# Kernel tuning notes

Hardware: AMD Instinct MI355X
Metric: run time of the kernel (lower is better)

Reference implementation:

```python
import jax, jax.numpy as jnp
import numpy as np

N = 65536   # voxels
K = 27      # 3x3x3 kernel offsets
LOG_P = float(np.log(101.0))  # Hmax = log(num img channels)
EPS_BN = 1e-5


def bn(x, p):
    # p: [4, C] = (gamma, beta, running_mean, running_var); eval-mode batchnorm
    g, b, m, v = p[0], p[1], p[2], p[3]
    return g * (x - m) * jax.lax.rsqrt(v + EPS_BN) + b


def spconv(x, nbr, W):
    # sparse 3^3 conv as gather-GEMM: x [N,Cin], nbr [N,K] int, W [K,Cin,Cout]
    g = x[nbr]                       # [N, K, Cin] irregular gather
    return jnp.einsum('nkc,kcd->nd', g, W)


def setup_inputs() -> dict:
    key = jax.random.key(0)
    ks = jax.random.split(key, 24)
    inp = {
        'feats': jax.random.uniform(ks[0], (N, 105), dtype=jnp.float32),
        'nbr1': jax.random.randint(ks[1], (N, K), 0, N, dtype=jnp.int32),
        'nbr2': jax.random.randint(ks[2], (N, K), 0, N, dtype=jnp.int32),
        'w_rgb': jax.random.normal(ks[3], (4, 32), jnp.float32) * 0.1,
        'b_rgb': jax.random.normal(ks[4], (32,), jnp.float32) * 0.1,
        'bn_rgb': jax.random.uniform(ks[5], (4, 32), dtype=jnp.float32),
        'w_img': jax.random.normal(ks[6], (101, 32), jnp.float32) * 0.1,
        'b_img': jax.random.normal(ks[7], (32,), jnp.float32) * 0.1,
        'bn_img': jax.random.uniform(ks[8], (4, 32), dtype=jnp.float32),
        'w_e1': jax.random.normal(ks[9], (K, 64, 96), jnp.float32) * 0.05,
        'w_e2': jax.random.normal(ks[10], (K, 96, 96), jnp.float32) * 0.05,
        'bn_e1': jax.random.uniform(ks[11], (4, 96), dtype=jnp.float32),
        'bn_e2': jax.random.uniform(ks[12], (4, 96), dtype=jnp.float32),
        'w_lab': jax.random.normal(ks[13], (96, 19), jnp.float32) * 0.1,
        'w_unlab': jax.random.normal(ks[14], (5, 96, 5), jnp.float32) * 0.1,
        'w_over': jax.random.normal(ks[15], (5, 96, 15), jnp.float32) * 0.1,
        'w_clip1': jax.random.normal(ks[16], (96, 256), jnp.float32) * 0.1,
        'b_clip1': jax.random.normal(ks[17], (256,), jnp.float32) * 0.1,
        'bn_clip': jax.random.uniform(ks[18], (4, 256), dtype=jnp.float32),
        'w_clip2': jax.random.normal(ks[19], (256, 512), jnp.float32) * 0.1,
        'b_clip2': jax.random.normal(ks[20], (512,), jnp.float32) * 0.1,
    }
    return inp


def reference(feats, nbr1, nbr2, w_rgb, b_rgb, bn_rgb, w_img, b_img, bn_img,
              w_e1, w_e2, bn_e1, bn_e2, w_lab, w_unlab, w_over,
              w_clip1, b_clip1, bn_clip, w_clip2, b_clip2):
    rgbi = feats[:, :4]
    p = feats[:, 4:]
    # entropy gate (computed under no_grad in the original)
    p_safe = jnp.clip(p, 1e-12, None)
    H = -(p_safe * jnp.log(p_safe)).sum(axis=1, keepdims=True)
    w = jax.lax.stop_gradient(1.0 - H / LOG_P)
    p_gate = p * w  # eval mode: no dropout
    # 1x1 sparse convs = per-voxel matmuls
    rgb32 = jax.nn.relu(bn(rgbi @ w_rgb + b_rgb, bn_rgb))
    img32 = jax.nn.relu(bn(p_gate @ w_img + b_img, bn_img))
    x = jnp.concatenate([rgb32, img32], axis=1)  # [N, 64]
    # encoder: gather-GEMM sparse 3^3 convs (MinkUNet body pattern), 64->96->96
    x = jax.nn.relu(bn(spconv(x, nbr1, w_e1), bn_e1))
    x = jax.nn.relu(bn(spconv(x, nbr2, w_e2), bn_e2))  # [N, 96] = feats
    # prototype heads (1x1 convs, bias-free)
    logits_lab = x @ w_lab                                 # [N, 19]
    logits_unlab = jnp.einsum('nc,hcp->hnp', x, w_unlab)   # [5, N, 5]
    logits_over = jnp.einsum('nc,hcp->hnp', x, w_over)     # [5, N, 15]
    # clip projector
    h = jax.nn.relu(bn(x @ w_clip1 + b_clip1, bn_clip))
    clip_feats = h @ w_clip2 + b_clip2                     # [N, 512]
    return (logits_lab, logits_unlab, logits_over, x, clip_feats)
```

## Files before the change

### kernel.cpp

```cpp
#include <hip/hip_runtime.h>
#include <math.h>

#define NNODES 65536
#define KNBR 27
#define EPS_BN 1e-5f
#define LOG_P 4.6151205168412597f

typedef float f32x4 __attribute__((ext_vector_type(4)));
typedef short s16x8 __attribute__((ext_vector_type(8)));

__device__ __forceinline__ unsigned short f2bf(float f) {
    union { float f; unsigned int u; } v; v.f = f;
    unsigned int u = v.u;
    unsigned int r = (u + 0x7fffu + ((u >> 16) & 1u)) >> 16;
    return (unsigned short)r;
}

__device__ __forceinline__ void gload16(const void* g, void* l) {
    __builtin_amdgcn_global_load_lds(
        (const __attribute__((address_space(1))) void*)g,
        (__attribute__((address_space(3))) void*)l, 16, 0, 0);
}

__global__ __launch_bounds__(256) void prep_w_kernel(
    const float* __restrict__ W, unsigned short* __restrict__ wpre, int CIN, int NCH)
{
    const int idx = blockIdx.x * 256 + threadIdx.x;
    const int total = KNBR * 96 * NCH * 8;
    if (idx >= total) return;
    const int e  = idx & 7;
    const int t1 = idx >> 3;
    const int ci = t1 % NCH;
    const int t2 = t1 / NCH;
    const int r  = t2 % 96;
    const int k  = t2 / 96;
    const int cc  = ci ^ (r & (NCH - 1));
    const int cin = cc * 8 + e;
    float v = (cin < CIN) ? W[((size_t)k * CIN + cin) * 96 + r] : 0.f;
    wpre[idx] = f2bf(v);
}

__global__ __launch_bounds__(256) void prep_wc1h_kernel(
    const float* __restrict__ w_clip1, const float* __restrict__ w_lab,
    const float* __restrict__ w_unlab, const float* __restrict__ w_over,
    unsigned short* __restrict__ out)
{
    const int idx = blockIdx.x * 256 + threadIdx.x;
    if (idx >= 3 * 384 * 32) return;
    const int e   = idx & 7;
    const int p2  = (idx >> 3) & 3;
    const int col = (idx >> 5) % 384;
    const int kt  = (idx >> 5) / 384;
    const int cin = (kt * 4 + (p2 ^ ((col >> 2) & 3))) * 8 + e;
    float v;
    if (col < 256)      v = w_clip1[(size_t)cin * 256 + col];
    else if (col < 275) v = w_lab[(size_t)cin * 19 + (col - 256)];
    else if (col < 300) { int jj = col - 275, hh = jj / 5,  p = jj - hh * 5;  v = w_unlab[((size_t)hh * 96 + cin) * 5  + p]; }
    else if (col < 375) { int jj = col - 300, hh = jj / 15, p = jj - hh * 15; v = w_over [((size_t)hh * 96 + cin) * 15 + p]; }
    else v = 0.f;
    out[idx] = f2bf(v);
}

__global__ __launch_bounds__(256) void prep_wc2_kernel(
    const float* __restrict__ w_clip2, unsigned short* __restrict__ out)
{
    const int idx = blockIdx.x * 256 + threadIdx.x;
    const int e   = idx & 7;
    const int p2  = (idx >> 3) & 3;
    const int col = (idx >> 5) & 511;
    const int kt  = idx >> 14;
    const int cin = (kt * 4 + (p2 ^ ((col >> 2) & 3))) * 8 + e;
    out[idx] = f2bf(w_clip2[(size_t)cin * 512 + col]);
}

__global__ __launch_bounds__(256) void stage1_kernel(
    const float* __restrict__ feats,
    const float* __restrict__ w_rgb, const float* __restrict__ b_rgb, const float* __restrict__ bn_rgb,
    const float* __restrict__ w_img, const float* __restrict__ b_img, const float* __restrict__ bn_img,
    unsigned short* __restrict__ x64b)
{
    __shared__ float s_f[4][106];
    const int wid  = threadIdx.x >> 6;
    const int lane = threadIdx.x & 63;
    const int n = blockIdx.x * 4 + wid;
    const float* fr = feats + (size_t)n * 105;
    for (int i = lane; i < 105; i += 64) s_f[wid][i] = fr[i];
    __syncthreads();

    float s = 0.f;
    for (int i = lane; i < 101; i += 64) {
        float pv = s_f[wid][4 + i];
        float ps = fmaxf(pv, 1e-12f);
        s += ps * logf(ps);
    }
    #pragma unroll
    for (int off = 32; off > 0; off >>= 1) s += __shfl_xor(s, off, 64);
    const float wgt = 1.0f + s * (1.0f / LOG_P);

    if (lane < 32) {
        const int j = lane;
        float acc = b_rgb[j];
        #pragma unroll
        for (int c = 0; c < 4; ++c) acc += s_f[wid][c] * w_rgb[c*32 + j];
        float y = bn_rgb[j] * (acc - bn_rgb[64+j]) * rsqrtf(bn_rgb[96+j] + EPS_BN) + bn_rgb[32+j];
        x64b[(size_t)n*64 + j] = f2bf(fmaxf(y, 0.f));
    } else {
        const int j = lane - 32;
        float acc = 0.f;
        for (int c = 0; c < 101; ++c) acc += s_f[wid][4+c] * w_img[c*32 + j];
        acc = acc * wgt + b_img[j];
        float y = bn_img[j] * (acc - bn_img[64+j]) * rsqrtf(bn_img[96+j] + EPS_BN) + bn_img[32+j];
        x64b[(size_t)n*64 + 32 + j] = f2bf(fmaxf(y, 0.f));
    }
}

template<int CIN, bool OUTBF>
__global__ __launch_bounds__(256, 2) void spconv_mfma(
    const char* __restrict__ xinb,
    const int*  __restrict__ nbr,
    const char* __restrict__ wpre,
    const float* __restrict__ bnp,
    float* __restrict__ outf,
    unsigned short* __restrict__ outb)
{
    constexpr int KT   = CIN / 32;
    constexpr int NCH  = (CIN == 96) ? 16 : 8;
    constexpr int CM   = NCH - 1;
    constexpr int ROWB = NCH * 16;
    constexpr int STG  = (96 * ROWB) / 4096;

    __shared__ int s_nbr[128 * KNBR];
    __shared__ __align__(16) char s_b[2][96 * ROWB];

    const int t   = threadIdx.x;
    const int wid = t >> 6;
    const int l   = t & 63;
    const int l15 = l & 15;
    const int l4  = l >> 4;
    const int n0  = blockIdx.x * 128;

    for (int i = t; i < 128 * KNBR; i += 256) s_nbr[i] = nbr[(size_t)n0 * KNBR + i];

    f32x4 acc[2][6];
    #pragma unroll
    for (int mt = 0; mt < 2; ++mt)
        #pragma unroll
        for (int nt = 0; nt < 6; ++nt) acc[mt][nt] = (f32x4){0.f, 0.f, 0.f, 0.f};

    float sc[6], mb[6], bb[6];
    #pragma unroll
    for (int nt = 0; nt < 6; ++nt) {
        const int d = nt * 16 + l15;
        sc[nt] = bnp[d] * rsqrtf(bnp[288 + d] + EPS_BN);
        mb[nt] = bnp[192 + d];
        bb[nt] = bnp[96 + d];
    }

    s16x8 a0[2][KT], a1[2][KT], a2r[2][KT];

#define STAGE(kk) do {                                                         \
    const char* _src = wpre + (size_t)(kk) * (96 * ROWB);                      \
    char* _dst = &s_b[(kk) & 1][0];                                            \
    _Pragma("unroll")                                                          \
    for (int _i = 0; _i < STG; ++_i)                                           \
        gload16(_src + _i * 4096 + t * 16, _dst + _i * 4096 + (wid << 10));    \
} while (0)

#define PRE(areg, kk) do {                                                     \
    _Pragma("unroll")                                                          \
    for (int _mt = 0; _mt < 2; ++_mt) {                                        \
        const int _nb = s_nbr[(wid * 32 + _mt * 16 + l15) * KNBR + (kk)];      \
        const char* _rp = xinb + (size_t)_nb * (CIN * 2) + (l4 << 4);          \
        _Pragma("unroll")                                                      \
        for (int _kt = 0; _kt < KT; ++_kt)                                     \
            areg[_mt][_kt] = *(const s16x8*)(_rp + _kt * 64);                  \
    }                                                                          \
} while (0)

#define COMP(areg, kk) do {                                                    \
    const char* _bb = &s_b[(kk) & 1][0];                                       \
    _Pragma("unroll")                                                          \
    for (int _kt = 0; _kt < KT; ++_kt) {                                       \
        s16x8 _bf[6];                                                          \
        _Pragma("unroll")                                                      \
        for (int _nt = 0; _nt < 6; ++_nt) {                                    \
            const int _row = _nt * 16 + l15;                                   \
            const int _c   = _kt * 4 + l4;                                     \
            _bf[_nt] = *(const s16x8*)(_bb + _row * ROWB + ((_c ^ (_row & CM)) << 4)); \
        }                                                                      \
        _Pragma("unroll")                                                      \
        for (int _nt = 0; _nt < 6; ++_nt) {                                    \
            acc[0][_nt] = __builtin_amdgcn_mfma_f32_16x16x32_bf16(areg[0][_kt], _bf[_nt], acc[0][_nt], 0, 0, 0); \
            acc[1][_nt] = __builtin_amdgcn_mfma_f32_16x16x32_bf16(areg[1][_kt], _bf[_nt], acc[1][_nt], 0, 0, 0); \
        }                                                                      \
    }                                                                          \
} while (0)

    __syncthreads();
    PRE(a0, 0);
    PRE(a1, 1);
    STAGE(0);
    __syncthreads();

    for (int k = 0; k < 27; k += 3) {
        STAGE(k + 1);
        PRE(a2r, k + 2);
        COMP(a0, k);
        __syncthreads();
        STAGE(k + 2);
        if (k + 3 < 27) PRE(a0, k + 3);
        COMP(a1, k + 1);
        __syncthreads();
        if (k + 3 < 27) STAGE(k + 3);
        if (k + 4 < 27) PRE(a1, k + 4);
        COMP(a2r, k + 2);
        __syncthreads();
    }

#undef STAGE
#undef PRE
#undef COMP

    #pragma unroll
    for (int mt = 0; mt < 2; ++mt)
        #pragma unroll
        for (int nt = 0; nt < 6; ++nt) {
            const int d = nt * 16 + l15;
            #pragma unroll
            for (int q = 0; q < 4; ++q) {
                const int node = n0 + wid * 32 + mt * 16 + l4 * 4 + q;
                float y = sc[nt] * (acc[mt][nt][q] - mb[nt]) + bb[nt];
                y = fmaxf(y, 0.f);
                if (OUTBF) outb[(size_t)node * 96 + d] = f2bf(y);
                else       outf[(size_t)node * 96 + d] = y;
            }
        }
}

__global__ __launch_bounds__(512, 2) void fused_clip_heads(
    const float* __restrict__ x,
    const char* __restrict__ wc1h,
    const char* __restrict__ wc2,
    const float* __restrict__ b_clip1, const float* __restrict__ bn_clip,
    const float* __restrict__ b_clip2,
    float* __restrict__ out_lab, float* __restrict__ out_unlab, float* __restrict__ out_over,
    float* __restrict__ outc)
{
    extern __shared__ __align__(16) char lds[];
    char* reg0 = lds;
    char* s_h  = lds + 65536;

    const int t   = threadIdx.x;
    const int wid = t >> 6;
    const int l   = t & 63;
    const int l15 = l & 15;
    const int l4  = l >> 4;
    const int wm  = wid >> 2;
    const int wn  = wid & 3;
    const int r0  = blockIdx.x * 128;

#define STG1(kt) do {                                                          \
    const char* _s = wc1h + (size_t)(kt) * 24576;                              \
    char* _d = reg0 + ((kt) & 1) * 32768;                                      \
    _Pragma("unroll")                                                          \
    for (int _i = 0; _i < 3; ++_i)                                             \
        gload16(_s + _i * 8192 + t * 16, _d + _i * 8192 + (wid << 10));        \
} while (0)

#define STG2(kt) do {                                                          \
    const char* _s = wc2 + (size_t)(kt) * 32768;                               \
    char* _d = reg0 + ((kt) & 1) * 32768;                                      \
    _Pragma("unroll")                                                          \
    for (int _i = 0; _i < 4; ++_i)                                             \
        gload16(_s + _i * 8192 + t * 16, _d + _i * 8192 + (wid << 10));        \
} while (0)

    STG1(0);

    s16x8 af[3][4];
    #pragma unroll
    for (int kt = 0; kt < 3; ++kt)
        #pragma unroll
        for (int mt = 0; mt < 4; ++mt) {
            const int r = r0 + wm*64 + mt*16 + l15;
            const float* bp = x + (size_t)r*96 + kt*32 + l4*8;
            const float4 xa = *(const float4*)bp;
            const float4 xb = *(const float4*)(bp + 4);
            s16x8 v;
            v[0]=(short)f2bf(xa.x); v[1]=(short)f2bf(xa.y); v[2]=(short)f2bf(xa.z); v[3]=(short)f2bf(xa.w);
            v[4]=(short)f2bf(xb.x); v[5]=(short)f2bf(xb.y); v[6]=(short)f2bf(xb.z); v[7]=(short)f2bf(xb.w);
            af[kt][mt] = v;
        }

    f32x4 acc1[4][6];
    #pragma unroll
    for (int mt = 0; mt < 4; ++mt)
        #pragma unroll
        for (int nt = 0; nt < 6; ++nt) acc1[mt][nt] = (f32x4){0.f,0.f,0.f,0.f};

    __syncthreads();

    for (int kt = 0; kt < 3; ++kt) {
        if (kt < 2) STG1(kt + 1);
        const char* buf = reg0 + (kt & 1) * 32768;
        s16x8 bf[6];
        #pragma unroll
        for (int nt = 0; nt < 6; ++nt) {
            const int col = wn*96 + nt*16 + l15;
            bf[nt] = *(const s16x8*)(buf + col*64 + ((l4 ^ ((col >> 2) & 3)) << 4));
        }
        #pragma unroll
        for (int nt = 0; nt < 6; ++nt)
            #pragma unroll
            for (int mt = 0; mt < 4; ++mt)
                acc1[mt][nt] = __builtin_amdgcn_mfma_f32_16x16x32_bf16(af[kt][mt], bf[nt], acc1[mt][nt], 0, 0, 0);
        __syncthreads();
    }

    STG2(0);

    #pragma unroll
    for (int nt = 0; nt < 6; ++nt) {
        const int j = wn*96 + nt*16 + l15;
        if (j < 256) {
            const float sc = bn_clip[j] * rsqrtf(bn_clip[768 + j] + EPS_BN);
            const float mb = bn_clip[512 + j];
            const float bb = bn_clip[256 + j];
            const float bias = b_clip1[j];
            const int c = j >> 3, e = j & 7;
            #pragma unroll
            for (int mt = 0; mt < 4; ++mt)
                #pragma unroll
                for (int q = 0; q < 4; ++q) {
                    const int row = wm*64 + mt*16 + l4*4 + q;
                    float y = fmaxf(sc * (acc1[mt][nt][q] + bias - mb) + bb, 0.f);
                    *(unsigned short*)(s_h + row*512 + ((c ^ (row & 31)) << 4) + e*2) = f2bf(y);
                }
        } else if (j < 375) {
            const int jh = j - 256;
            #pragma unroll
            for (int mt = 0; mt < 4; ++mt)
                #pragma unroll
                for (int q = 0; q < 4; ++q) {
                    const int n = r0 + wm*64 + mt*16 + l4*4 + q;
                    const float v = acc1[mt][nt][q];
                    if (jh < 19)      out_lab[(size_t)n*19 + jh] = v;
                    else if (jh < 44) { int jj = jh-19, hh = jj/5,  p = jj-hh*5;  out_unlab[((size_t)hh*NNODES + n)*5  + p] = v; }
                    else              { int jj = jh-44, hh = jj/15, p = jj-hh*15; out_over [((size_t)hh*NNODES + n)*15 + p] = v; }
                }
        }
    }
    __syncthreads();

    f32x4 acc2[4][8];
    #pragma unroll
    for (int mt = 0; mt < 4; ++mt)
        #pragma unroll
        for (int nt = 0; nt < 8; ++nt) acc2[mt][nt] = (f32x4){0.f,0.f,0.f,0.f};

    for (int kt = 0; kt < 8; ++kt) {
        if (kt < 7) STG2(kt + 1);
        const char* buf = reg0 + (kt & 1) * 32768;
        s16x8 a2[4];
        #pragma unroll
        for (int mt = 0; mt < 4; ++mt) {
            const int row = wm*64 + mt*16 + l15;
            a2[mt] = *(const s16x8*)(s_h + row*512 + (((kt*4 + l4) ^ (row & 31)) << 4));
        }
        s16x8 b2[8];
        #pragma unroll
        for (int nt = 0; nt < 8; ++nt) {
            const int col = wn*128 + nt*16 + l15;
            b2[nt] = *(const s16x8*)(buf + col*64 + ((l4 ^ ((col >> 2) & 3)) << 4));
        }
        #pragma unroll
        for (int nt = 0; nt < 8; ++nt)
            #pragma unroll
            for (int mt = 0; mt < 4; ++mt)
                acc2[mt][nt] = __builtin_amdgcn_mfma_f32_16x16x32_bf16(a2[mt], b2[nt], acc2[mt][nt], 0, 0, 0);
        __syncthreads();
    }
#undef STG1
#undef STG2

    #pragma unroll
    for (int nt = 0; nt < 8; ++nt) {
        const int col = wn*128 + nt*16 + l15;
        const float bb = b_clip2[col];
        #pragma unroll
        for (int mt = 0; mt < 4; ++mt)
            #pragma unroll
            for (int q = 0; q < 4; ++q) {
                const int row = wm*64 + mt*16 + l4*4 + q;
                outc[(size_t)(r0 + row)*512 + col] = acc2[mt][nt][q] + bb;
            }
    }
}

extern "C" void kernel_launch(void* const* d_in, const int* in_sizes, int n_in,
                              void* d_out, int out_size, void* d_ws, size_t ws_size,
                              hipStream_t stream)
{
    const float* feats   = (const float*)d_in[0];
    const int*   nbr1    = (const int*)  d_in[1];
    const int*   nbr2    = (const int*)  d_in[2];
    const float* w_rgb   = (const float*)d_in[3];
    const float* b_rgb   = (const float*)d_in[4];
    const float* bn_rgb  = (const float*)d_in[5];
    const float* w_img   = (const float*)d_in[6];
    const float* b_img   = (const float*)d_in[7];
    const float* bn_img  = (const float*)d_in[8];
    const float* w_e1    = (const float*)d_in[9];
    const float* w_e2    = (const float*)d_in[10];
    const float* bn_e1   = (const float*)d_in[11];
    const float* bn_e2   = (const float*)d_in[12];
    const float* w_lab   = (const float*)d_in[13];
    const float* w_unlab = (const float*)d_in[14];
    const float* w_over  = (const float*)d_in[15];
    const float* w_clip1 = (const float*)d_in[16];
    const float* b_clip1 = (const float*)d_in[17];
    const float* bn_clip = (const float*)d_in[18];
    const float* w_clip2 = (const float*)d_in[19];
    const float* b_clip2 = (const float*)d_in[20];

    float* out = (float*)d_out;
    const size_t off_unlab = (size_t)NNODES * 19;
    const size_t off_over  = (size_t)NNODES * 44;
    const size_t off_x     = (size_t)NNODES * 119;
    const size_t off_clip  = (size_t)NNODES * 215;

    char* scratch = (char*)(out + off_clip);
    unsigned short* x64b  = (unsigned short*)scratch;
    unsigned short* x96b  = (unsigned short*)(scratch + (8u << 20));
    unsigned short* wpre1 = (unsigned short*)(scratch + (21u << 20));
    unsigned short* wpre2 = (unsigned short*)(scratch + (22u << 20));

    char* wc1h = (char*)d_ws;
    char* wc2  = (char*)d_ws + 73728;

    prep_w_kernel<<<(KNBR*96*8*8  + 255) / 256, 256, 0, stream>>>(w_e1, wpre1, 64, 8);
    prep_w_kernel<<<(KNBR*96*16*8 + 255) / 256, 256, 0, stream>>>(w_e2, wpre2, 96, 16);
    prep_wc1h_kernel<<<(3*384*32 + 255) / 256, 256, 0, stream>>>(w_clip1, w_lab, w_unlab, w_over,
                                                                 (unsigned short*)wc1h);
    prep_wc2_kernel<<<131072 / 256, 256, 0, stream>>>(w_clip2, (unsigned short*)wc2);

    stage1_kernel<<<NNODES/4, 256, 0, stream>>>(feats, w_rgb, b_rgb, bn_rgb, w_img, b_img, bn_img, x64b);

    spconv_mfma<64, true ><<<NNODES/128, 256, 0, stream>>>((const char*)x64b, nbr1, (const char*)wpre1,
                                                           bn_e1, nullptr, x96b);
    spconv_mfma<96, false><<<NNODES/128, 256, 0, stream>>>((const char*)x96b, nbr2, (const char*)wpre2,
                                                           bn_e2, out + off_x, nullptr);

    fused_clip_heads<<<NNODES/128, 512, 131072, stream>>>(
        out + off_x, wc1h, wc2, b_clip1, bn_clip, b_clip2,
        out, out + off_unlab, out + off_over, out + off_clip);
}
```

Before: 252.4 us.

## Halve spconv rows per wave, drop LDS neighbor table, raise occupancy

Each wave in the sparse-conv kernels now covers 16 voxels instead of 32, so a block handles 64 rows and twice as many blocks are launched. The LDS neighbor-index table is removed and each PRE reads its index straight from global memory. BN constants are now loaded in the epilogue instead of being held in registers, and launch bounds allow 3 blocks per CU. The smaller register and LDS footprint is meant to raise occupancy and hide gather latency. In exchange, each staged weight tile in LDS is reused by half as many rows, which doubles weight staging traffic per voxel.

```diff
diff --git a/kernel.cpp b/kernel.cpp
--- a/kernel.cpp
+++ b/kernel.cpp
@@ -115,7 +115,7 @@
 }
 
 template<int CIN, bool OUTBF>
-__global__ __launch_bounds__(256, 2) void spconv_mfma(
+__global__ __launch_bounds__(256, 3) void spconv_mfma(
     const char* __restrict__ xinb,
     const int*  __restrict__ nbr,
     const char* __restrict__ wpre,
@@ -129,7 +129,6 @@
     constexpr int ROWB = NCH * 16;
     constexpr int STG  = (96 * ROWB) / 4096;
 
-    __shared__ int s_nbr[128 * KNBR];
     __shared__ __align__(16) char s_b[2][96 * ROWB];
 
     const int t   = threadIdx.x;
@@ -137,26 +136,14 @@
     const int l   = t & 63;
     const int l15 = l & 15;
     const int l4  = l >> 4;
-    const int n0  = blockIdx.x * 128;
-
-    for (int i = t; i < 128 * KNBR; i += 256) s_nbr[i] = nbr[(size_t)n0 * KNBR + i];
-
-    f32x4 acc[2][6];
-    #pragma unroll
-    for (int mt = 0; mt < 2; ++mt)
-        #pragma unroll
-        for (int nt = 0; nt < 6; ++nt) acc[mt][nt] = (f32x4){0.f, 0.f, 0.f, 0.f};
-
-    float sc[6], mb[6], bb[6];
-    #pragma unroll
-    for (int nt = 0; nt < 6; ++nt) {
-        const int d = nt * 16 + l15;
-        sc[nt] = bnp[d] * rsqrtf(bnp[288 + d] + EPS_BN);
-        mb[nt] = bnp[192 + d];
-        bb[nt] = bnp[96 + d];
-    }
-
-    s16x8 a0[2][KT], a1[2][KT], a2r[2][KT];
+    const int n0  = blockIdx.x * 64;
+    const size_t nbase = (size_t)(n0 + wid * 16 + l15) * KNBR;
+
+    f32x4 acc[6];
+    #pragma unroll
+    for (int nt = 0; nt < 6; ++nt) acc[nt] = (f32x4){0.f, 0.f, 0.f, 0.f};
+
+    s16x8 a0[KT], a1[KT], a2r[KT];
 
 #define STAGE(kk) do {                                                         \
     const char* _src = wpre + (size_t)(kk) * (96 * ROWB);                      \
@@ -167,14 +154,11 @@
 } while (0)
 
 #define PRE(areg, kk) do {                                                     \
+    const int _nb = nbr[nbase + (kk)];                                         \
+    const char* _rp = xinb + (size_t)_nb * (CIN * 2) + (l4 << 4);              \
     _Pragma("unroll")                                                          \
-    for (int _mt = 0; _mt < 2; ++_mt) {                                        \
-        const int _nb = s_nbr[(wid * 32 + _mt * 16 + l15) * KNBR + (kk)];      \
-        const char* _rp = xinb + (size_t)_nb * (CIN * 2) + (l4 << 4);          \
-        _Pragma("unroll")                                                      \
-        for (int _kt = 0; _kt < KT; ++_kt)                                     \
-            areg[_mt][_kt] = *(const s16x8*)(_rp + _kt * 64);                  \
-    }                                                                          \
+    for (int _kt = 0; _kt < KT; ++_kt)                                         \
+        areg[_kt] = *(const s16x8*)(_rp + _kt * 64);                           \
 } while (0)
 
 #define COMP(areg, kk) do {                                                    \
@@ -189,14 +173,11 @@
             _bf[_nt] = *(const s16x8*)(_bb + _row * ROWB + ((_c ^ (_row & CM)) << 4)); \
         }                                                                      \
         _Pragma("unroll")                                                      \
-        for (int _nt = 0; _nt < 6; ++_nt) {                                    \
-            acc[0][_nt] = __builtin_amdgcn_mfma_f32_16x16x32_bf16(areg[0][_kt], _bf[_nt], acc[0][_nt], 0, 0, 0); \
-            acc[1][_nt] = __builtin_amdgcn_mfma_f32_16x16x32_bf16(areg[1][_kt], _bf[_nt], acc[1][_nt], 0, 0, 0); \
-        }                                                                      \
+        for (int _nt = 0; _nt < 6; ++_nt)                                      \
+            acc[_nt] = __builtin_amdgcn_mfma_f32_16x16x32_bf16(areg[_kt], _bf[_nt], acc[_nt], 0, 0, 0); \
     }                                                                          \
 } while (0)
 
-    __syncthreads();
     PRE(a0, 0);
     PRE(a1, 1);
     STAGE(0);
@@ -222,19 +203,20 @@
 #undef COMP
 
     #pragma unroll
-    for (int mt = 0; mt < 2; ++mt)
-        #pragma unroll
-        for (int nt = 0; nt < 6; ++nt) {
-            const int d = nt * 16 + l15;
-            #pragma unroll
-            for (int q = 0; q < 4; ++q) {
-                const int node = n0 + wid * 32 + mt * 16 + l4 * 4 + q;
-                float y = sc[nt] * (acc[mt][nt][q] - mb[nt]) + bb[nt];
-                y = fmaxf(y, 0.f);
-                if (OUTBF) outb[(size_t)node * 96 + d] = f2bf(y);
-                else       outf[(size_t)node * 96 + d] = y;
-            }
-        }
+    for (int nt = 0; nt < 6; ++nt) {
+        const int d = nt * 16 + l15;
+        const float sc = bnp[d] * rsqrtf(bnp[288 + d] + EPS_BN);
+        const float mb = bnp[192 + d];
+        const float bb = bnp[96 + d];
+        #pragma unroll
+        for (int q = 0; q < 4; ++q) {
+            const int node = n0 + wid * 16 + l4 * 4 + q;
+            float y = sc * (acc[nt][q] - mb) + bb;
+            y = fmaxf(y, 0.f);
+            if (OUTBF) outb[(size_t)node * 96 + d] = f2bf(y);
+            else       outf[(size_t)node * 96 + d] = y;
+        }
+    }
 }
 
 __global__ __launch_bounds__(512, 2) void fused_clip_heads(
@@ -446,10 +428,10 @@
 
     stage1_kernel<<<NNODES/4, 256, 0, stream>>>(feats, w_rgb, b_rgb, bn_rgb, w_img, b_img, bn_img, x64b);
 
-    spconv_mfma<64, true ><<<NNODES/128, 256, 0, stream>>>((const char*)x64b, nbr1, (const char*)wpre1,
-                                                           bn_e1, nullptr, x96b);
-    spconv_mfma<96, false><<<NNODES/128, 256, 0, stream>>>((const char*)x96b, nbr2, (const char*)wpre2,
-                                                           bn_e2, out + off_x, nullptr);
+    spconv_mfma<64, true ><<<NNODES/64, 256, 0, stream>>>((const char*)x64b, nbr1, (const char*)wpre1,
+                                                          bn_e1, nullptr, x96b);
+    spconv_mfma<96, false><<<NNODES/64, 256, 0, stream>>>((const char*)x96b, nbr2, (const char*)wpre2,
+                                                          bn_e2, out + off_x, nullptr);
 
     fused_clip_heads<<<NNODES/128, 512, 131072, stream>>>(
         out + off_x, wc1h, wc2, b_clip1, bn_clip, b_clip2,
```

Result: slower. 263.9 us (+4.6%).

## Replace full barriers with partial vmcnt waits and peel final gather-GEMM iterations

Applied to the files above, without the earlier changes.

In the sparse-conv gather-GEMM loop, each __syncthreads is replaced by a barrier that waits only on older vector-memory ops (vmcnt 6 or 4). In-flight prefetches of later neighbour rows and weight stages can then stay outstanding across the barrier. The last three k-steps are peeled out so the loop body carries no conditionals, and batchnorm parameter loads move into the epilogue to free registers during the main loop. This relies on the hand-counted vmcnt matching the compiler's actual load ordering; a wrong count would race on LDS or registers.

```diff
diff --git a/kernel.cpp b/kernel.cpp
--- a/kernel.cpp
+++ b/kernel.cpp
@@ -147,15 +147,6 @@
         #pragma unroll
         for (int nt = 0; nt < 6; ++nt) acc[mt][nt] = (f32x4){0.f, 0.f, 0.f, 0.f};
 
-    float sc[6], mb[6], bb[6];
-    #pragma unroll
-    for (int nt = 0; nt < 6; ++nt) {
-        const int d = nt * 16 + l15;
-        sc[nt] = bnp[d] * rsqrtf(bnp[288 + d] + EPS_BN);
-        mb[nt] = bnp[192 + d];
-        bb[nt] = bnp[96 + d];
-    }
-
     s16x8 a0[2][KT], a1[2][KT], a2r[2][KT];
 
 #define STAGE(kk) do {                                                         \
@@ -164,6 +155,7 @@
     _Pragma("unroll")                                                          \
     for (int _i = 0; _i < STG; ++_i)                                           \
         gload16(_src + _i * 4096 + t * 16, _dst + _i * 4096 + (wid << 10));    \
+    asm volatile("" ::: "memory");                                             \
 } while (0)
 
 #define PRE(areg, kk) do {                                                     \
@@ -196,40 +188,59 @@
     }                                                                          \
 } while (0)
 
+#define KBAR() do {                                                            \
+    if (KT == 3) asm volatile("s_waitcnt vmcnt(6)" ::: "memory");              \
+    else         asm volatile("s_waitcnt vmcnt(4)" ::: "memory");              \
+    __builtin_amdgcn_s_barrier();                                              \
+} while (0)
+
     __syncthreads();
     PRE(a0, 0);
     PRE(a1, 1);
     STAGE(0);
     __syncthreads();
 
-    for (int k = 0; k < 27; k += 3) {
+    for (int k = 0; k < 24; k += 3) {
         STAGE(k + 1);
         PRE(a2r, k + 2);
         COMP(a0, k);
-        __syncthreads();
+        KBAR();
         STAGE(k + 2);
-        if (k + 3 < 27) PRE(a0, k + 3);
+        PRE(a0, k + 3);
         COMP(a1, k + 1);
-        __syncthreads();
-        if (k + 3 < 27) STAGE(k + 3);
-        if (k + 4 < 27) PRE(a1, k + 4);
+        KBAR();
+        STAGE(k + 3);
+        PRE(a1, k + 4);
         COMP(a2r, k + 2);
-        __syncthreads();
-    }
+        KBAR();
+    }
+    STAGE(25);
+    PRE(a2r, 26);
+    COMP(a0, 24);
+    KBAR();
+    STAGE(26);
+    COMP(a1, 25);
+    asm volatile("s_waitcnt vmcnt(0)" ::: "memory");
+    __builtin_amdgcn_s_barrier();
+    COMP(a2r, 26);
 
 #undef STAGE
 #undef PRE
 #undef COMP
+#undef KBAR
 
     #pragma unroll
     for (int mt = 0; mt < 2; ++mt)
         #pragma unroll
         for (int nt = 0; nt < 6; ++nt) {
             const int d = nt * 16 + l15;
+            const float sc = bnp[d] * rsqrtf(bnp[288 + d] + EPS_BN);
+            const float mb = bnp[192 + d];
+            const float bb = bnp[96 + d];
             #pragma unroll
             for (int q = 0; q < 4; ++q) {
                 const int node = n0 + wid * 32 + mt * 16 + l4 * 4 + q;
-                float y = sc[nt] * (acc[mt][nt][q] - mb[nt]) + bb[nt];
+                float y = sc * (acc[mt][nt][q] - mb) + bb;
                 y = fmaxf(y, 0.f);
                 if (OUTBF) outb[(size_t)node * 96 + d] = f2bf(y);
                 else       outf[(size_t)node * 96 + d] = y;
```

Result: faster. 241.4 us (-4.3%).
